# Kernel tuning notes

Hardware: AMD Instinct MI355X
Metric: run time of the kernel (lower is better)

The kernel has to match this reference:

```python
import jax, jax.numpy as jnp
import numpy as np

IMAGE_SIZE = 800
OUT = 50          # feature map size
FEAT = 512
SCALES = (2.0, 4.0, 6.0)
RATIOS = (0.5, 1.0, 1.5)
A = len(SCALES) * len(RATIOS)          # 9 anchors per cell
POS_THR, NEG_THR = 0.7, 0.3
W_CONF, W_REG = 1.0, 5.0
SCALE = IMAGE_SIZE // OUT              # 16, stride of feature map


def _anchor_base():
    # order: ratio outer loop, scale inner loop (matches get_anchor_base)
    ws = jnp.array([s * r for r in RATIOS for s in SCALES], jnp.float32)  # [A]
    hs = jnp.array([s for r in RATIOS for s in SCALES], jnp.float32)      # [A]
    cx = (jnp.arange(OUT, dtype=jnp.float32) + 0.5)[:, None, None]        # grid dim0 -> x
    cy = (jnp.arange(OUT, dtype=jnp.float32) + 0.5)[None, :, None]        # grid dim1 -> y
    xmin = jnp.clip(cx - ws / 2, 0.0, OUT)
    xmax = jnp.clip(cx + ws / 2, 0.0, OUT)
    ymin = jnp.clip(cy - hs / 2, 0.0, OUT)
    ymax = jnp.clip(cy + hs / 2, 0.0, OUT)
    shp = (OUT, OUT, A)
    base = jnp.stack([jnp.broadcast_to(xmin, shp), jnp.broadcast_to(ymin, shp),
                      jnp.broadcast_to(xmax, shp), jnp.broadcast_to(ymax, shp)], axis=-1)
    return base.reshape(-1, 4)         # [N,4], N = OUT*OUT*A = 22500


def _iou(anchors, gt):
    # anchors [N,4], gt [B,M,4] (xyxy) -> iou [B,N,M]
    a = anchors[None, :, None, :]
    g = gt[:, None, :, :]
    ix1 = jnp.maximum(a[..., 0], g[..., 0]); iy1 = jnp.maximum(a[..., 1], g[..., 1])
    ix2 = jnp.minimum(a[..., 2], g[..., 2]); iy2 = jnp.minimum(a[..., 3], g[..., 3])
    inter = jnp.clip(ix2 - ix1, 0.0) * jnp.clip(iy2 - iy1, 0.0)
    area_a = (a[..., 2] - a[..., 0]) * (a[..., 3] - a[..., 1])
    area_g = (g[..., 2] - g[..., 0]) * (g[..., 3] - g[..., 1])
    return inter / (area_a + area_g - inter + 1e-8)


def _smooth_l1(d):
    ad = jnp.abs(d)
    return jnp.where(ad < 1.0, 0.5 * d * d, ad - 0.5)


def setup_inputs() -> dict:
    key = jax.random.key(0)
    ks = jax.random.split(key, 8)
    B, M = 16, 16
    features = jax.random.normal(ks[0], (B, FEAT, OUT, OUT), jnp.float32)
    # valid GT boxes in image coords: centers in [100,700], sizes in [32,200]
    cxy = jax.random.uniform(ks[1], (B, M, 2), jnp.float32, 100.0, 700.0)
    wh = jax.random.uniform(ks[2], (B, M, 2), jnp.float32, 32.0, 200.0)
    x1y1 = jnp.clip(cxy - wh / 2, 0.0, IMAGE_SIZE)
    x2y2 = jnp.clip(cxy + wh / 2, 0.0, IMAGE_SIZE)
    gt_boxes = jnp.concatenate([x1y1, x2y2], axis=-1)
    w1 = jax.random.normal(ks[3], (FEAT, FEAT, 3, 3), jnp.float32) * 0.02
    b1 = jnp.zeros((FEAT,), jnp.float32)
    w_cls = jax.random.normal(ks[4], (A, FEAT), jnp.float32) * 0.02
    b_cls = jnp.zeros((A,), jnp.float32)
    w_box = jax.random.normal(ks[5], (4 * A, FEAT), jnp.float32) * 0.02
    b_box = jnp.zeros((4 * A,), jnp.float32)
    return {"features": features, "gt_boxes": gt_boxes, "w1": w1, "b1": b1,
            "w_cls": w_cls, "b_cls": b_cls, "w_box": w_box, "b_box": b_box}


def reference(features, gt_boxes, w1, b1, w_cls, b_cls, w_box, b_box):
    B = features.shape[0]
    anchors = _anchor_base()                                   # [N,4]
    N = anchors.shape[0]

    # --- conv tower ---
    x = jax.lax.conv_general_dilated(features, w1, (1, 1), 'SAME') + b1[None, :, None, None]
    cls_map = jnp.einsum('bchw,ac->bahw', x, w_cls) + b_cls[None, :, None, None]   # [B,A,H,W]
    box_map = jnp.einsum('bchw,dc->bdhw', x, w_box) + b_box[None, :, None, None]   # [B,4A,H,W]
    logits = jnp.transpose(cls_map, (0, 2, 3, 1)).reshape(B, N)                    # [B,N]
    pred_off = jnp.transpose(box_map.reshape(B, A, 4, OUT, OUT), (0, 3, 4, 1, 2)).reshape(B, N, 4)

    # --- project gt to feature-map (anchor) coords, 'p2a' ---
    gt = gt_boxes / SCALE                                       # [B,M,4]

    # --- anchor/GT assignment ---
    iou = _iou(anchors, gt)                                     # [B,N,M]
    max_per_gt = jnp.max(iou, axis=1, keepdims=True)            # best anchor per gt
    pos_mask = ((iou == max_per_gt) & (max_per_gt > 0)) | (iou > POS_THR)  # [B,N,M]
    pos_mask = pos_mask.astype(jnp.float32)
    n_pos = jnp.maximum(pos_mask.sum(), 1.0)

    # --- gt offsets (standard tx,ty,tw,th) for every (anchor,gt) pair ---
    acx = (anchors[:, 0] + anchors[:, 2]) / 2
    acy = (anchors[:, 1] + anchors[:, 3]) / 2
    aw = jnp.maximum(anchors[:, 2] - anchors[:, 0], 1e-6)
    ah = jnp.maximum(anchors[:, 3] - anchors[:, 1], 1e-6)
    gcx = (gt[..., 0] + gt[..., 2]) / 2                         # [B,M]
    gcy = (gt[..., 1] + gt[..., 3]) / 2
    gw = jnp.maximum(gt[..., 2] - gt[..., 0], 1e-6)
    gh = jnp.maximum(gt[..., 3] - gt[..., 1], 1e-6)
    tx = (gcx[:, None, :] - acx[None, :, None]) / aw[None, :, None]   # [B,N,M]
    ty = (gcy[:, None, :] - acy[None, :, None]) / ah[None, :, None]
    tw = jnp.log(gw[:, None, :] / aw[None, :, None])
    th = jnp.log(gh[:, None, :] / ah[None, :, None])
    gt_off = jnp.stack([tx, ty, tw, th], axis=-1)               # [B,N,M,4]

    diff = gt_off - pred_off[:, :, None, :]
    reg_loss = (pos_mask[..., None] * _smooth_l1(diff)).sum() / (4.0 * n_pos)

    # --- classification loss: BCE-with-logits; positives=1, negatives=0 ---
    pos_loss = (pos_mask * jax.nn.softplus(-logits)[:, :, None]).sum() / n_pos
    neg_anchor = jnp.all(iou < NEG_THR, axis=2).astype(jnp.float32)   # [B,N]
    n_neg = jnp.maximum(neg_anchor.sum(), 1.0)
    neg_loss = (neg_anchor * jax.nn.softplus(logits)).sum() / n_neg
    cls_loss = 0.5 * (pos_loss + neg_loss)

    total_rpn_loss = W_CONF * cls_loss + W_REG * reg_loss

    # --- proposals from predicted offsets for all anchors ---
    pcx = acx[None, :] + pred_off[..., 0] * aw[None, :]
    pcy = acy[None, :] + pred_off[..., 1] * ah[None, :]
    pw = aw[None, :] * jnp.exp(pred_off[..., 2])
    ph = ah[None, :] * jnp.exp(pred_off[..., 3])
    proposals = jnp.stack([pcx - pw / 2, pcy - ph / 2, pcx + pw / 2, pcy + ph / 2], axis=-1)  # [B,N,4]

    return total_rpn_loss, proposals
```

## Files before the change

kernel.cpp:

```cpp
#include <hip/hip_runtime.h>
#include <hip/hip_bf16.h>
#include <stdint.h>


using bf16x8 = __attribute__((ext_vector_type(8))) __bf16;
using f32x4  = __attribute__((ext_vector_type(4))) float;

#define FT_CHUNK_STRIDE 2768896
#define W2_CHUNK_B 27648

__device__ __forceinline__ unsigned short f2bf(float f) {
  union { float f; unsigned u; } x; x.f = f;
  unsigned r = x.u + 0x7fffu + ((x.u >> 16) & 1u);
  return (unsigned short)(r >> 16);
}

__device__ __forceinline__ void gl_lds16(const void* g, void* l) {
  __builtin_amdgcn_global_load_lds(
      (const __attribute__((address_space(1))) void*)g,
      (__attribute__((address_space(3))) void*)l, 16, 0, 0);
}

__device__ __forceinline__ float sl1(float d) {
  float ad = fabsf(d);
  return ad < 1.f ? 0.5f * d * d : ad - 0.5f;
}
__device__ __forceinline__ float softplus_f(float x) {
  return fmaxf(x, 0.f) + log1pf(expf(-fabsf(x)));
}

__device__ __forceinline__ void anchor_strict(int n, float& ax1, float& ay1,
                                              float& ax2, float& ay2) {
  int ii = n / 450;
  int rem = n - ii * 450;
  int jj = rem / 9;
  int a  = rem - jj * 9;
  const float SC[3] = {2.f, 4.f, 6.f};
  const float RA[3] = {0.5f, 1.f, 1.5f};
  float w = __fmul_rn(SC[a % 3], RA[a / 3]);
  float h = SC[a % 3];
  float cx = __fadd_rn((float)ii, 0.5f);
  float cy = __fadd_rn((float)jj, 0.5f);
  float wh = __fmul_rn(w, 0.5f), hh = __fmul_rn(h, 0.5f);
  ax1 = fminf(fmaxf(__fsub_rn(cx, wh), 0.f), 50.f);
  ax2 = fminf(fmaxf(__fadd_rn(cx, wh), 0.f), 50.f);
  ay1 = fminf(fmaxf(__fsub_rn(cy, hh), 0.f), 50.f);
  ay2 = fminf(fmaxf(__fadd_rn(cy, hh), 0.f), 50.f);
}
__device__ __forceinline__ float iou_pre(float ax1, float ay1, float ax2, float ay2,
                                         float aarea, const float* __restrict__ s) {
  float ix1 = fmaxf(ax1, s[0]), iy1 = fmaxf(ay1, s[1]);
  float ix2 = fminf(ax2, s[2]), iy2 = fminf(ay2, s[3]);
  float inter = __fmul_rn(fmaxf(__fsub_rn(ix2, ix1), 0.f),
                          fmaxf(__fsub_rn(iy2, iy1), 0.f));
  float denom = __fadd_rn(__fsub_rn(__fadd_rn(aarea, s[4]), inter), 1e-8f);
  return __fdiv_rn(inter, denom);
}
__device__ __forceinline__ float iou_strict(float ax1, float ay1, float ax2, float ay2,
                                            float aarea, const float* __restrict__ g) {
  float s[5];
  s[0] = __fmul_rn(g[0], 0.0625f); s[1] = __fmul_rn(g[1], 0.0625f);
  s[2] = __fmul_rn(g[2], 0.0625f); s[3] = __fmul_rn(g[3], 0.0625f);
  s[4] = __fmul_rn(__fsub_rn(s[2], s[0]), __fsub_rn(s[3], s[1]));
  return iou_pre(ax1, ay1, ax2, ay2, aarea, s);
}

__global__ __launch_bounds__(256, 4) void k1(const float* __restrict__ feat,
                                             char* __restrict__ featT2,
                                             const float* __restrict__ w1,
                                             const float* __restrict__ wc,
                                             const float* __restrict__ wb,
                                             const float* __restrict__ b1,
                                             const float* __restrict__ bc,
                                             const float* __restrict__ bbx,
                                             float* __restrict__ part,
                                             float* __restrict__ bias_eff,
                                             const float* __restrict__ gt_boxes,
                                             unsigned* __restrict__ mx,
                                             unsigned* __restrict__ accz) {
  __shared__ __align__(16) char smem[64 * 132 * 2];
  const int bxr = blockIdx.x;
  const int tid = threadIdx.x;

  if (bxr < 576) {
    if (bxr == 0 && tid < 8) accz[tid] = 0u;
    int cz = bxr / 72, kx = bxr - cz * 72;
    float* sW = (float*)smem;
#pragma unroll
    for (int q = 0; q < 12; ++q) {
      int idx = tid + q * 256;
      int co = idx >> 6, cl = idx & 63;
      int c = cz * 64 + cl;
      float v = 0.f;
      if (co < 9) v = wc[co * 512 + c];
      else if (co < 45) v = wb[(co - 9) * 512 + c];
      sW[co * 64 + cl] = v;
    }
    __syncthreads();
    const int kmem = kx * 64 + (tid & 63);
    const int coq  = tid >> 6;
    float acc[12];
#pragma unroll
    for (int j = 0; j < 12; ++j) acc[j] = 0.f;
    const float* w1p = w1 + (size_t)(cz * 64) * 4608 + kmem;
    for (int c4 = 0; c4 < 64; c4 += 4) {
      float f0 = w1p[(size_t)(c4 + 0) * 4608];
      float f1 = w1p[(size_t)(c4 + 1) * 4608];
      float f2 = w1p[(size_t)(c4 + 2) * 4608];
      float f3 = w1p[(size_t)(c4 + 3) * 4608];
#pragma unroll
      for (int j = 0; j < 12; ++j) {
        float4 wv = *(const float4*)&sW[(coq * 12 + j) * 64 + c4];
        acc[j] += wv.x * f0 + wv.y * f1 + wv.z * f2 + wv.w * f3;
      }
    }
    float* dst = part + (size_t)cz * 221184 + kmem;
#pragma unroll
    for (int j = 0; j < 12; ++j) dst[(size_t)(coq * 12 + j) * 4608] = acc[j];
    return;
  }

  if (bxr < 624) {
    int co = bxr - 576;
    int l = tid;
    if (l >= 64) return;
    float s = 0.f;
#pragma unroll
    for (int q = 0; q < 8; ++q) {
      int c = q * 64 + l;
      float wv = co < 9 ? wc[co * 512 + c] : (co < 45 ? wb[(co - 9) * 512 + c] : 0.f);
      s += wv * b1[c];
    }
    for (int o = 32; o; o >>= 1) s += __shfl_down(s, o, 64);
    if (l == 0)
      bias_eff[co] = s + (co < 9 ? bc[co] : (co < 45 ? bbx[co - 9] : 0.f));
    return;
  }

  if (bxr < 880) {
    int q = bxr - 624;
    int b = q >> 4, m = q & 15;
    const float* g = gt_boxes + (b * 16 + m) * 4;
    float s[5];
    s[0] = __fmul_rn(g[0], 0.0625f); s[1] = __fmul_rn(g[1], 0.0625f);
    s[2] = __fmul_rn(g[2], 0.0625f); s[3] = __fmul_rn(g[3], 0.0625f);
    s[4] = __fmul_rn(__fsub_rn(s[2], s[0]), __fsub_rn(s[3], s[1]));
    float best = 0.f;
    for (int n = tid; n < 22500; n += 256) {
      float ax1, ay1, ax2, ay2;
      anchor_strict(n, ax1, ay1, ax2, ay2);
      float aarea = __fmul_rn(__fsub_rn(ax2, ax1), __fsub_rn(ay2, ay1));
      best = fmaxf(best, iou_pre(ax1, ay1, ax2, ay2, aarea, s));
    }
    for (int o = 32; o; o >>= 1) best = fmaxf(best, __shfl_down(best, o, 64));
    float* red = (float*)smem;
    if ((tid & 63) == 0) red[tid >> 6] = best;
    __syncthreads();
    if (tid == 0) {
      float v = fmaxf(fmaxf(red[0], red[1]), fmaxf(red[2], red[3]));
      mx[b * 16 + m] = __float_as_uint(v);
    }
    return;
  }

  const int bxr2 = bxr - 880;
  const int tile = bxr2 % 41;
  const int rest = bxr2 / 41;
  const int g    = rest & 3;
  const int b    = rest >> 2;
  if (tile == 40) {
    uint4 z = {0, 0, 0, 0};
    for (int u = tid; u < 204 * 4; u += 256) {
      int p = u & 255; if (p >= 204) p -= 204;
      int c4 = u / 204;
      int ip, jp;
      if (p < 52)       { ip = 0;       jp = p; }
      else if (p < 104) { ip = 51;      jp = p - 52; }
      else if (p < 154) { ip = p - 103; jp = 0; }
      else              { ip = p - 153; jp = 51; }
      char* dst = featT2 + (size_t)(g * 4 + c4) * FT_CHUNK_STRIDE
                + (size_t)(b * 2704 + ip * 52 + jp) * 64;
      *(uint4*)(dst)      = z;
      *(uint4*)(dst + 16) = z;
      *(uint4*)(dst + 32) = z;
      *(uint4*)(dst + 48) = z;
    }
    return;
  }
  unsigned short* sT = (unsigned short*)smem;
  const int pos0 = tile * 64;
  const float* fb = feat + (size_t)b * 1280000 + (size_t)(g * 128) * 2500;
  const int pq = tid & 15;
  const int cq = tid >> 4;
  const int p  = pos0 + pq * 4;
  float vv[2][4][4];
  if (p + 3 < 2500) {
#pragma unroll
    for (int it = 0; it < 2; ++it)
#pragma unroll
      for (int q = 0; q < 4; ++q) {
        float4 v = *(const float4*)(fb + (size_t)(it * 64 + cq * 4 + q) * 2500 + p);
        vv[it][q][0] = v.x; vv[it][q][1] = v.y;
        vv[it][q][2] = v.z; vv[it][q][3] = v.w;
      }
  } else {
#pragma unroll
    for (int it = 0; it < 2; ++it)
#pragma unroll
      for (int q = 0; q < 4; ++q)
#pragma unroll
        for (int e = 0; e < 4; ++e)
          vv[it][q][e] = fb[(size_t)(it * 64 + cq * 4 + q) * 2500 + min(p + e, 2499)];
  }
#pragma unroll
  for (int it = 0; it < 2; ++it) {
#pragma unroll
    for (int pp = 0; pp < 4; ++pp) {
      ushort4 pk;
      pk.x = f2bf(vv[it][0][pp]); pk.y = f2bf(vv[it][1][pp]);
      pk.z = f2bf(vv[it][2][pp]); pk.w = f2bf(vv[it][3][pp]);
      *(ushort4*)&sT[(pq * 4 + pp) * 132 + it * 64 + cq * 4] = pk;
    }
  }
  __syncthreads();
  {
    int ch = tid >> 6, pr = tid & 63;
    int gp = pos0 + pr;
    if (gp < 2500) {
      int i = gp / 50, j = gp - i * 50;
      char* dst = featT2 + (size_t)(g * 4 + ch) * FT_CHUNK_STRIDE
                + (size_t)(b * 2704 + (i + 1) * 52 + (j + 1)) * 64;
      const uint4* src = (const uint4*)&sT[pr * 132 + ch * 32];
      uint4 a0 = src[0], a1 = src[1], a2 = src[2], a3 = src[3];
      *(uint4*)(dst)      = a0;
      *(uint4*)(dst + 16) = a1;
      *(uint4*)(dst + 32) = a2;
      *(uint4*)(dst + 48) = a3;
    }
  }
}

__global__ __launch_bounds__(256) void k2(const float* __restrict__ part,
                                          unsigned short* __restrict__ w2) {
  int co = blockIdx.x / 18, kx = blockIdx.x - co * 18;
  int kmem = kx * 256 + threadIdx.x;
  const float* p = part + (size_t)co * 4608 + kmem;
  float s = 0.f;
#pragma unroll
  for (int cz = 0; cz < 8; ++cz) s += p[(size_t)cz * 221184];
  int ci = kmem / 9, tap = kmem - ci * 9;
  int c = ci >> 5, e = ci & 31;
  int boff = c * W2_CHUNK_B + tap * 3072 + (co >> 4) * 1024 + (co & 15) * 64
           + ((((e >> 3) ^ co) & 3) << 4) + ((e & 7) << 1);
  w2[boff >> 1] = f2bf(s);
}

__global__ __launch_bounds__(256, 2) void k3(const char* __restrict__ featT2,
                                             const char* __restrict__ w2g,
                                             const float* __restrict__ beff,
                                             float* __restrict__ oh) {
  __shared__ __align__(16) char sF[2][11264];
  __shared__ __align__(16) char sA[2][27648];
  const int tid = threadIdx.x, lane = tid & 63, w = tid >> 6;
  const int bx0 = blockIdx.x;
  const int bx = ((bx0 & 7) << 6) | (bx0 >> 3);
  const int b = bx >> 5, tl = bx & 31, tr = tl >> 3, tc = tl & 7;
  const int i0 = tr * 13 - (tr == 3 ? 1 : 0);
  const int TI = (tr >= 2) ? 12 : 13;
  const int TJ = (tc < 2) ? 7 : 6;
  const int j0 = (tc < 2) ? tc * 7 : 14 + (tc - 2) * 6;
  const int TJ2 = TJ + 2;
  const int mcount = TI * TJ;
  const int pieces = (TI + 2) * TJ2 * 5;

  const char* srcF[3];
#pragma unroll
  for (int k = 0; k < 3; ++k) {
    int s = w * 3 + k;
    int pi = s * 64 + lane;
    if (pi >= pieces) pi = pieces - 1;
    int pos = pi / 5, pc = pi - pos * 5;
    if (pc > 3) pc = 3;
    int hi = pos / TJ2, hj = pos - hi * TJ2;
    srcF[k] = featT2 + (size_t)(b * 2704 + (i0 + hi) * 52 + (j0 + hj)) * 64 + pc * 16;
  }
  int idxB[2];
#pragma unroll
  for (int bf = 0; bf < 2; ++bf) {
    int p = (w * 2 + bf) * 16 + (lane & 15);
    if (p >= mcount) p = mcount - 1;
    int di = p / TJ, dj = p - di * TJ;
    idxB[bf] = (di * TJ2 + dj) * 80 + (lane >> 4) * 16;
  }
  const int aoff = (lane & 15) * 64 + ((((lane >> 4) ^ lane) & 3) << 4);
  int toff[9];
#pragma unroll
  for (int tp = 0; tp < 9; ++tp) toff[tp] = ((tp / 3) * TJ2 + (tp % 3)) * 80;

  f32x4 acc[3][2] = {};

  auto stage = [&](int c, int pb) {
    size_t coff = (size_t)c * FT_CHUNK_STRIDE;
#pragma unroll
    for (int k = 0; k < 3; ++k) {
      int s = w * 3 + k;
      if (s < 11) gl_lds16(srcF[k] + coff, sF[pb] + s * 1024);
    }
#pragma unroll
    for (int k = 0; k < 7; ++k) {
      int s = w + 4 * k;
      if (s < 27)
        gl_lds16(w2g + (size_t)c * W2_CHUNK_B + s * 1024 + lane * 16, sA[pb] + s * 1024);
    }
  };

  stage(0, 0);
  __builtin_amdgcn_s_waitcnt(0);
  __syncthreads();

  for (int c = 0; c < 16; ++c) {
    int pb = c & 1;
    if (c < 15) stage(c + 1, pb ^ 1);
    const char* fA = sA[pb];
    const char* fB = sF[pb];
#pragma unroll
    for (int tp = 0; tp < 9; ++tp) {
      bf16x8 av[3], bv[2];
#pragma unroll
      for (int cf = 0; cf < 3; ++cf)
        av[cf] = *(const bf16x8*)(fA + tp * 3072 + cf * 1024 + aoff);
#pragma unroll
      for (int bf = 0; bf < 2; ++bf)
        bv[bf] = *(const bf16x8*)(fB + idxB[bf] + toff[tp]);
#pragma unroll
      for (int cf = 0; cf < 3; ++cf)
#pragma unroll
        for (int bf = 0; bf < 2; ++bf)
          acc[cf][bf] = __builtin_amdgcn_mfma_f32_16x16x32_bf16(av[cf], bv[bf], acc[cf][bf], 0, 0, 0);
    }
    __builtin_amdgcn_s_waitcnt(0);
    __syncthreads();
  }

  f32x4 bias[3];
#pragma unroll
  for (int cf = 0; cf < 3; ++cf)
    bias[cf] = *(const f32x4*)(beff + cf * 16 + (lane >> 4) * 4);
#pragma unroll
  for (int bf = 0; bf < 2; ++bf) {
    int p = (w * 2 + bf) * 16 + (lane & 15);
    if (p >= mcount) continue;
    int di = p / TJ, dj = p - di * TJ;
    int gm = (b * 50 + i0 + di) * 50 + (j0 + dj);
#pragma unroll
    for (int cf = 0; cf < 3; ++cf) {
      f32x4 v = acc[cf][bf];
#pragma unroll
      for (int r = 0; r < 4; ++r) v[r] += bias[cf][r];
      *(f32x4*)(oh + (size_t)gm * 48 + cf * 16 + (lane >> 4) * 4) = v;
    }
  }
}

__global__ __launch_bounds__(256) void k4(const float* __restrict__ gt_boxes,
                                          const unsigned* __restrict__ mxbuf,
                                          const float* __restrict__ oh,
                                          float* __restrict__ accum,
                                          float* __restrict__ dout) {
  const int tid = threadIdx.x;
  const int b = blockIdx.y;
  __shared__ float sg[16][10];
  if (tid < 16) {
    const float* g = gt_boxes + (b * 16 + tid) * 4;
    float gx1 = __fmul_rn(g[0], 0.0625f), gy1 = __fmul_rn(g[1], 0.0625f);
    float gx2 = __fmul_rn(g[2], 0.0625f), gy2 = __fmul_rn(g[3], 0.0625f);
    sg[tid][0] = gx1; sg[tid][1] = gy1; sg[tid][2] = gx2; sg[tid][3] = gy2;
    sg[tid][4] = __fmul_rn(__fsub_rn(gx2, gx1), __fsub_rn(gy2, gy1));
    sg[tid][5] = (gx1 + gx2) * 0.5f;
    sg[tid][6] = (gy1 + gy2) * 0.5f;
    sg[tid][7] = fmaxf(gx2 - gx1, 1e-6f);
    sg[tid][8] = fmaxf(gy2 - gy1, 1e-6f);
  }
  __syncthreads();

  const int n0 = blockIdx.x * 512 + tid;
  const int n1 = n0 + 256;
  const bool vA = n0 < 22500, vB = n1 < 22500;
  float s_np = 0.f, s_reg = 0.f, s_pos = 0.f, s_nc = 0.f, s_nl = 0.f;

  float Aax1 = 0, Aay1 = 0, Aax2 = 0, Aay2 = 0, Aarea = 0, Aacx = 0, Aacy = 0,
        Aaw = 1, Aah = 1, Alog = 0, Ap0 = 0, Ap1 = 0, Ap2 = 0, Ap3 = 0;
  float Bax1 = 0, Bay1 = 0, Bax2 = 0, Bay2 = 0, Barea = 0, Bacx = 0, Bacy = 0,
        Baw = 1, Bah = 1, Blog = 0, Bp0 = 0, Bp1 = 0, Bp2 = 0, Bp3 = 0;
  int npA = 0, npB = 0;
  bool anA = true, anB = true;

  if (vA) {
    anchor_strict(n0, Aax1, Aay1, Aax2, Aay2);
    Aarea = __fmul_rn(__fsub_rn(Aax2, Aax1), __fsub_rn(Aay2, Aay1));
    Aacx = (Aax1 + Aax2) * 0.5f; Aacy = (Aay1 + Aay2) * 0.5f;
    Aaw = fmaxf(Aax2 - Aax1, 1e-6f); Aah = fmaxf(Aay2 - Aay1, 1e-6f);
    int ii = n0 / 450, rem = n0 - ii * 450, jj = rem / 9, a = rem - jj * 9;
    const float* row = oh + ((size_t)(b * 2500 + ii * 50 + jj)) * 48;
    Alog = row[a];
    Ap0 = row[9 + a * 4]; Ap1 = row[10 + a * 4];
    Ap2 = row[11 + a * 4]; Ap3 = row[12 + a * 4];
  }
  if (vB) {
    anchor_strict(n1, Bax1, Bay1, Bax2, Bay2);
    Barea = __fmul_rn(__fsub_rn(Bax2, Bax1), __fsub_rn(Bay2, Bay1));
    Bacx = (Bax1 + Bax2) * 0.5f; Bacy = (Bay1 + Bay2) * 0.5f;
    Baw = fmaxf(Bax2 - Bax1, 1e-6f); Bah = fmaxf(Bay2 - Bay1, 1e-6f);
    int ii = n1 / 450, rem = n1 - ii * 450, jj = rem / 9, a = rem - jj * 9;
    const float* row = oh + ((size_t)(b * 2500 + ii * 50 + jj)) * 48;
    Blog = row[a];
    Bp0 = row[9 + a * 4]; Bp1 = row[10 + a * 4];
    Bp2 = row[11 + a * 4]; Bp3 = row[12 + a * 4];
  }

#pragma unroll
  for (int m = 0; m < 16; ++m) {
    const float* s = sg[m];
    float mxv = __uint_as_float(mxbuf[b * 16 + m]);
    float iouA = vA ? iou_pre(Aax1, Aay1, Aax2, Aay2, Aarea, s) : 0.f;
    float iouB = vB ? iou_pre(Bax1, Bay1, Bax2, Bay2, Barea, s) : 0.f;
    if (vA) {
      bool pos = ((iouA == mxv) && (mxv > 0.f)) || (iouA > 0.7f);
      if (iouA >= 0.3f) anA = false;
      if (pos) {
        ++npA;
        float tx = (s[5] - Aacx) / Aaw, ty = (s[6] - Aacy) / Aah;
        float twv = logf(s[7] / Aaw), thv = logf(s[8] / Aah);
        s_reg += sl1(tx - Ap0) + sl1(ty - Ap1) + sl1(twv - Ap2) + sl1(thv - Ap3);
      }
    }
    if (vB) {
      bool pos = ((iouB == mxv) && (mxv > 0.f)) || (iouB > 0.7f);
      if (iouB >= 0.3f) anB = false;
      if (pos) {
        ++npB;
        float tx = (s[5] - Bacx) / Baw, ty = (s[6] - Bacy) / Bah;
        float twv = logf(s[7] / Baw), thv = logf(s[8] / Bah);
        s_reg += sl1(tx - Bp0) + sl1(ty - Bp1) + sl1(twv - Bp2) + sl1(thv - Bp3);
      }
    }
  }
  if (vA) {
    s_np += (float)npA;
    s_pos += (float)npA * softplus_f(-Alog);
    if (anA) { s_nc += 1.f; s_nl += softplus_f(Alog); }
    float pcx = Aacx + Ap0 * Aaw, pcy = Aacy + Ap1 * Aah;
    float pw = Aaw * expf(Ap2), ph = Aah * expf(Ap3);
    float* o = dout + 1 + ((size_t)b * 22500 + n0) * 4;
    o[0] = pcx - pw * 0.5f; o[1] = pcy - ph * 0.5f;
    o[2] = pcx + pw * 0.5f; o[3] = pcy + ph * 0.5f;
  }
  if (vB) {
    s_np += (float)npB;
    s_pos += (float)npB * softplus_f(-Blog);
    if (anB) { s_nc += 1.f; s_nl += softplus_f(Blog); }
    float pcx = Bacx + Bp0 * Baw, pcy = Bacy + Bp1 * Bah;
    float pw = Baw * expf(Bp2), ph = Bah * expf(Bp3);
    float* o = dout + 1 + ((size_t)b * 22500 + n1) * 4;
    o[0] = pcx - pw * 0.5f; o[1] = pcy - ph * 0.5f;
    o[2] = pcx + pw * 0.5f; o[3] = pcy + ph * 0.5f;
  }

  float vals[5] = {s_np, s_reg, s_pos, s_nc, s_nl};
  __shared__ float red[4][5];
#pragma unroll
  for (int q = 0; q < 5; ++q) {
    float v = vals[q];
    for (int o = 32; o; o >>= 1) v += __shfl_down(v, o, 64);
    if ((tid & 63) == 0) red[tid >> 6][q] = v;
  }
  __syncthreads();
  if (tid < 5) {
    float v = red[0][tid] + red[1][tid] + red[2][tid] + red[3][tid];
    atomicAdd(accum + tid, v);
  }
  __syncthreads();
  if (tid == 0) {
    __threadfence();
    unsigned old = atomicAdd((unsigned*)(accum + 5), 1u);
    if (old == 703u) {
      float np = fmaxf(atomicAdd(accum + 0, 0.f), 1.f);
      float rg = atomicAdd(accum + 1, 0.f);
      float pp = atomicAdd(accum + 2, 0.f);
      float nn = fmaxf(atomicAdd(accum + 3, 0.f), 1.f);
      float nl = atomicAdd(accum + 4, 0.f);
      dout[0] = 0.5f * (pp / np + nl / nn) + 5.f * (rg / (4.f * np));
    }
  }
}

extern "C" void kernel_launch(void* const* d_in, const int* in_sizes, int n_in,
                              void* d_out, int out_size, void* d_ws, size_t ws_size,
                              hipStream_t stream) {
  const float* features = (const float*)d_in[0];
  const float* gt_boxes = (const float*)d_in[1];
  const float* w1    = (const float*)d_in[2];
  const float* b1    = (const float*)d_in[3];
  const float* w_cls = (const float*)d_in[4];
  const float* b_cls = (const float*)d_in[5];
  const float* w_box = (const float*)d_in[6];
  const float* b_box = (const float*)d_in[7];
  float* out = (float*)d_out;
  char* ws = (char*)d_ws;

  char*           featT2 = ws;
  unsigned short* w2     = (unsigned short*)(ws + 44302336);
  float*          wpart  = (float*)(ws + 44855296);
  float*          oh     = (float*)(ws + 51933184);
  float*          beff   = (float*)(ws + 59613184);
  unsigned*       mx     = (unsigned*)(ws + 59613376);
  float*          accum  = (float*)(ws + 59614400);

  k1<<<3504, 256, 0, stream>>>(features, featT2, w1, w_cls, w_box, b1, b_cls,
                               b_box, wpart, beff, gt_boxes, mx,
                               (unsigned*)accum);
  k2<<<864, 256, 0, stream>>>(wpart, w2);
  k3<<<512, 256, 0, stream>>>(featT2, (const char*)w2, beff, oh);
  k4<<<dim3(44, 16), 256, 0, stream>>>(gt_boxes, mx, oh, accum, out);
}
```

Baseline: 238.1 us.

## Split feature transpose into separate kernel with direct register-to-global bf16 writes

```diff
diff --git a/kernel.cpp b/kernel.cpp
--- a/kernel.cpp
+++ b/kernel.cpp
@@ -56,36 +56,81 @@
   float denom = __fadd_rn(__fsub_rn(__fadd_rn(aarea, s[4]), inter), 1e-8f);
   return __fdiv_rn(inter, denom);
 }
-__device__ __forceinline__ float iou_strict(float ax1, float ay1, float ax2, float ay2,
-                                            float aarea, const float* __restrict__ g) {
-  float s[5];
-  s[0] = __fmul_rn(g[0], 0.0625f); s[1] = __fmul_rn(g[1], 0.0625f);
-  s[2] = __fmul_rn(g[2], 0.0625f); s[3] = __fmul_rn(g[3], 0.0625f);
-  s[4] = __fmul_rn(__fsub_rn(s[2], s[0]), __fsub_rn(s[3], s[1]));
-  return iou_pre(ax1, ay1, ax2, ay2, aarea, s);
-}
-
-__global__ __launch_bounds__(256, 4) void k1(const float* __restrict__ feat,
-                                             char* __restrict__ featT2,
-                                             const float* __restrict__ w1,
-                                             const float* __restrict__ wc,
-                                             const float* __restrict__ wb,
-                                             const float* __restrict__ b1,
-                                             const float* __restrict__ bc,
-                                             const float* __restrict__ bbx,
-                                             float* __restrict__ part,
-                                             float* __restrict__ bias_eff,
-                                             const float* __restrict__ gt_boxes,
-                                             unsigned* __restrict__ mx,
-                                             unsigned* __restrict__ accz) {
-  __shared__ __align__(16) char smem[64 * 132 * 2];
+
+__global__ __launch_bounds__(256, 4) void k1a(const float* __restrict__ feat,
+                                              char* __restrict__ featT2) {
+  const int bx = blockIdx.x;
+  const int tid = threadIdx.x;
+  if (bx >= 768) {
+    int q = bx - 768;
+    int c = q & 15, b = q >> 4;
+    uint4 z = {0, 0, 0, 0};
+    for (int p = tid; p < 204; p += 256) {
+      int ip, jp;
+      if (p < 52)       { ip = 0;       jp = p; }
+      else if (p < 104) { ip = 51;      jp = p - 52; }
+      else if (p < 154) { ip = p - 103; jp = 0; }
+      else              { ip = p - 153; jp = 51; }
+      char* dst = featT2 + (size_t)c * FT_CHUNK_STRIDE
+                + (size_t)(b * 2704 + ip * 52 + jp) * 64;
+      *(uint4*)(dst)      = z;
+      *(uint4*)(dst + 16) = z;
+      *(uint4*)(dst + 32) = z;
+      *(uint4*)(dst + 48) = z;
+    }
+    return;
+  }
+  const int t = bx % 3, rest = bx / 3;
+  const int c = rest & 15, b = rest >> 4;
+  const int p0 = t * 1024 + tid * 4;
+  if (p0 >= 2500) return;
+  const float* fb = feat + (size_t)b * 1280000 + (size_t)(c * 32) * 2500 + p0;
+  char* d[4];
+#pragma unroll
+  for (int pp = 0; pp < 4; ++pp) {
+    int gp = p0 + pp;
+    int i = gp / 50, j = gp - i * 50;
+    d[pp] = featT2 + (size_t)c * FT_CHUNK_STRIDE
+          + (size_t)(b * 2704 + (i + 1) * 52 + (j + 1)) * 64;
+  }
+#pragma unroll
+  for (int h = 0; h < 2; ++h) {
+    float4 v[16];
+#pragma unroll
+    for (int q = 0; q < 16; ++q)
+      v[q] = *(const float4*)(fb + (size_t)(h * 16 + q) * 2500);
+#pragma unroll
+    for (int pp = 0; pp < 4; ++pp) {
+      unsigned short u[16];
+#pragma unroll
+      for (int q = 0; q < 16; ++q) {
+        float fv = pp == 0 ? v[q].x : pp == 1 ? v[q].y : pp == 2 ? v[q].z : v[q].w;
+        u[q] = f2bf(fv);
+      }
+      *(uint4*)(d[pp] + h * 32)      = *(uint4*)&u[0];
+      *(uint4*)(d[pp] + h * 32 + 16) = *(uint4*)&u[8];
+    }
+  }
+}
+
+__global__ __launch_bounds__(256, 4) void k1b(const float* __restrict__ w1,
+                                              const float* __restrict__ wc,
+                                              const float* __restrict__ wb,
+                                              const float* __restrict__ b1,
+                                              const float* __restrict__ bc,
+                                              const float* __restrict__ bbx,
+                                              float* __restrict__ part,
+                                              float* __restrict__ bias_eff,
+                                              const float* __restrict__ gt_boxes,
+                                              unsigned* __restrict__ mx,
+                                              unsigned* __restrict__ accz) {
+  __shared__ __align__(16) float sW[48 * 64];
   const int bxr = blockIdx.x;
   const int tid = threadIdx.x;
 
   if (bxr < 576) {
     if (bxr == 0 && tid < 8) accz[tid] = 0u;
     int cz = bxr / 72, kx = bxr - cz * 72;
-    float* sW = (float*)smem;
 #pragma unroll
     for (int q = 0; q < 12; ++q) {
       int idx = tid + q * 256;
@@ -137,7 +182,7 @@
     return;
   }
 
-  if (bxr < 880) {
+  {
     int q = bxr - 624;
     int b = q >> 4, m = q & 15;
     const float* g = gt_boxes + (b * 16 + m) * 4;
@@ -153,89 +198,11 @@
       best = fmaxf(best, iou_pre(ax1, ay1, ax2, ay2, aarea, s));
     }
     for (int o = 32; o; o >>= 1) best = fmaxf(best, __shfl_down(best, o, 64));
-    float* red = (float*)smem;
-    if ((tid & 63) == 0) red[tid >> 6] = best;
+    if ((tid & 63) == 0) sW[tid >> 6] = best;
     __syncthreads();
     if (tid == 0) {
-      float v = fmaxf(fmaxf(red[0], red[1]), fmaxf(red[2], red[3]));
+      float v = fmaxf(fmaxf(sW[0], sW[1]), fmaxf(sW[2], sW[3]));
       mx[b * 16 + m] = __float_as_uint(v);
-    }
-    return;
-  }
-
-  const int bxr2 = bxr - 880;
-  const int tile = bxr2 % 41;
-  const int rest = bxr2 / 41;
-  const int g    = rest & 3;
-  const int b    = rest >> 2;
-  if (tile == 40) {
-    uint4 z = {0, 0, 0, 0};
-    for (int u = tid; u < 204 * 4; u += 256) {
-      int p = u & 255; if (p >= 204) p -= 204;
-      int c4 = u / 204;
-      int ip, jp;
-      if (p < 52)       { ip = 0;       jp = p; }
-      else if (p < 104) { ip = 51;      jp = p - 52; }
-      else if (p < 154) { ip = p - 103; jp = 0; }
-      else              { ip = p - 153; jp = 51; }
-      char* dst = featT2 + (size_t)(g * 4 + c4) * FT_CHUNK_STRIDE
-                + (size_t)(b * 2704 + ip * 52 + jp) * 64;
-      *(uint4*)(dst)      = z;
-      *(uint4*)(dst + 16) = z;
-      *(uint4*)(dst + 32) = z;
-      *(uint4*)(dst + 48) = z;
-    }
-    return;
-  }
-  unsigned short* sT = (unsigned short*)smem;
-  const int pos0 = tile * 64;
-  const float* fb = feat + (size_t)b * 1280000 + (size_t)(g * 128) * 2500;
-  const int pq = tid & 15;
-  const int cq = tid >> 4;
-  const int p  = pos0 + pq * 4;
-  float vv[2][4][4];
-  if (p + 3 < 2500) {
-#pragma unroll
-    for (int it = 0; it < 2; ++it)
-#pragma unroll
-      for (int q = 0; q < 4; ++q) {
-        float4 v = *(const float4*)(fb + (size_t)(it * 64 + cq * 4 + q) * 2500 + p);
-        vv[it][q][0] = v.x; vv[it][q][1] = v.y;
-        vv[it][q][2] = v.z; vv[it][q][3] = v.w;
-      }
-  } else {
-#pragma unroll
-    for (int it = 0; it < 2; ++it)
-#pragma unroll
-      for (int q = 0; q < 4; ++q)
-#pragma unroll
-        for (int e = 0; e < 4; ++e)
-          vv[it][q][e] = fb[(size_t)(it * 64 + cq * 4 + q) * 2500 + min(p + e, 2499)];
-  }
-#pragma unroll
-  for (int it = 0; it < 2; ++it) {
-#pragma unroll
-    for (int pp = 0; pp < 4; ++pp) {
-      ushort4 pk;
-      pk.x = f2bf(vv[it][0][pp]); pk.y = f2bf(vv[it][1][pp]);
-      pk.z = f2bf(vv[it][2][pp]); pk.w = f2bf(vv[it][3][pp]);
-      *(ushort4*)&sT[(pq * 4 + pp) * 132 + it * 64 + cq * 4] = pk;
-    }
-  }
-  __syncthreads();
-  {
-    int ch = tid >> 6, pr = tid & 63;
-    int gp = pos0 + pr;
-    if (gp < 2500) {
-      int i = gp / 50, j = gp - i * 50;
-      char* dst = featT2 + (size_t)(g * 4 + ch) * FT_CHUNK_STRIDE
-                + (size_t)(b * 2704 + (i + 1) * 52 + (j + 1)) * 64;
-      const uint4* src = (const uint4*)&sT[pr * 132 + ch * 32];
-      uint4 a0 = src[0], a1 = src[1], a2 = src[2], a3 = src[3];
-      *(uint4*)(dst)      = a0;
-      *(uint4*)(dst + 16) = a1;
-      *(uint4*)(dst + 32) = a2;
-      *(uint4*)(dst + 48) = a3;
     }
   }
 }
@@ -516,10 +483,10 @@
   unsigned*       mx     = (unsigned*)(ws + 59613376);
   float*          accum  = (float*)(ws + 59614400);
 
-  k1<<<3504, 256, 0, stream>>>(features, featT2, w1, w_cls, w_box, b1, b_cls,
-                               b_box, wpart, beff, gt_boxes, mx,
-                               (unsigned*)accum);
+  k1b<<<880, 256, 0, stream>>>(w1, w_cls, w_box, b1, b_cls, b_box, wpart, beff,
+                               gt_boxes, mx, (unsigned*)accum);
   k2<<<864, 256, 0, stream>>>(wpart, w2);
+  k1a<<<1024, 256, 0, stream>>>(features, featT2);
   k3<<<512, 256, 0, stream>>>(featT2, (const char*)w2, beff, oh);
   k4<<<dim3(44, 16), 256, 0, stream>>>(gt_boxes, mx, oh, accum, out);
 }
```

New measurement: 270.4 us. +13.6%, slower.

## Split per-GT max-IoU search across anchor chunks with two-stage reduction

Applied to the files above, without the earlier changes.

```diff
diff --git a/kernel.cpp b/kernel.cpp
--- a/kernel.cpp
+++ b/kernel.cpp
@@ -56,14 +56,6 @@
   float denom = __fadd_rn(__fsub_rn(__fadd_rn(aarea, s[4]), inter), 1e-8f);
   return __fdiv_rn(inter, denom);
 }
-__device__ __forceinline__ float iou_strict(float ax1, float ay1, float ax2, float ay2,
-                                            float aarea, const float* __restrict__ g) {
-  float s[5];
-  s[0] = __fmul_rn(g[0], 0.0625f); s[1] = __fmul_rn(g[1], 0.0625f);
-  s[2] = __fmul_rn(g[2], 0.0625f); s[3] = __fmul_rn(g[3], 0.0625f);
-  s[4] = __fmul_rn(__fsub_rn(s[2], s[0]), __fsub_rn(s[3], s[1]));
-  return iou_pre(ax1, ay1, ax2, ay2, aarea, s);
-}
 
 __global__ __launch_bounds__(256, 4) void k1(const float* __restrict__ feat,
                                              char* __restrict__ featT2,
@@ -76,9 +68,9 @@
                                              float* __restrict__ part,
                                              float* __restrict__ bias_eff,
                                              const float* __restrict__ gt_boxes,
-                                             unsigned* __restrict__ mx,
+                                             float* __restrict__ mxPart,
                                              unsigned* __restrict__ accz) {
-  __shared__ __align__(16) char smem[64 * 132 * 2];
+  __shared__ __align__(16) char smem[16896];
   const int bxr = blockIdx.x;
   const int tid = threadIdx.x;
 
@@ -137,33 +129,47 @@
     return;
   }
 
-  if (bxr < 880) {
+  if (bxr < 2032) {
     int q = bxr - 624;
-    int b = q >> 4, m = q & 15;
-    const float* g = gt_boxes + (b * 16 + m) * 4;
-    float s[5];
-    s[0] = __fmul_rn(g[0], 0.0625f); s[1] = __fmul_rn(g[1], 0.0625f);
-    s[2] = __fmul_rn(g[2], 0.0625f); s[3] = __fmul_rn(g[3], 0.0625f);
-    s[4] = __fmul_rn(__fsub_rn(s[2], s[0]), __fsub_rn(s[3], s[1]));
-    float best = 0.f;
-    for (int n = tid; n < 22500; n += 256) {
+    int b = q / 88, nb = q - b * 88;
+    int n = nb * 256 + tid;
+    float (*sgg)[5] = (float(*)[5])smem;
+    float (*red)[16] = (float(*)[16])((float*)smem + 128);
+    if (tid < 16) {
+      const float* g = gt_boxes + (b * 16 + tid) * 4;
+      float gx1 = __fmul_rn(g[0], 0.0625f), gy1 = __fmul_rn(g[1], 0.0625f);
+      float gx2 = __fmul_rn(g[2], 0.0625f), gy2 = __fmul_rn(g[3], 0.0625f);
+      sgg[tid][0] = gx1; sgg[tid][1] = gy1; sgg[tid][2] = gx2; sgg[tid][3] = gy2;
+      sgg[tid][4] = __fmul_rn(__fsub_rn(gx2, gx1), __fsub_rn(gy2, gy1));
+    }
+    __syncthreads();
+    float lm[16];
+#pragma unroll
+    for (int m = 0; m < 16; ++m) lm[m] = 0.f;
+    if (n < 22500) {
       float ax1, ay1, ax2, ay2;
       anchor_strict(n, ax1, ay1, ax2, ay2);
       float aarea = __fmul_rn(__fsub_rn(ax2, ax1), __fsub_rn(ay2, ay1));
-      best = fmaxf(best, iou_pre(ax1, ay1, ax2, ay2, aarea, s));
-    }
-    for (int o = 32; o; o >>= 1) best = fmaxf(best, __shfl_down(best, o, 64));
-    float* red = (float*)smem;
-    if ((tid & 63) == 0) red[tid >> 6] = best;
+#pragma unroll
+      for (int m = 0; m < 16; ++m)
+        lm[m] = iou_pre(ax1, ay1, ax2, ay2, aarea, sgg[m]);
+    }
+#pragma unroll
+    for (int m = 0; m < 16; ++m) {
+      float v = lm[m];
+      for (int o = 32; o; o >>= 1) v = fmaxf(v, __shfl_down(v, o, 64));
+      if ((tid & 63) == 0) red[tid >> 6][m] = v;
+    }
     __syncthreads();
-    if (tid == 0) {
-      float v = fmaxf(fmaxf(red[0], red[1]), fmaxf(red[2], red[3]));
-      mx[b * 16 + m] = __float_as_uint(v);
+    if (tid < 16) {
+      float v = fmaxf(fmaxf(red[0][tid], red[1][tid]),
+                      fmaxf(red[2][tid], red[3][tid]));
+      mxPart[(b * 16 + tid) * 88 + nb] = v;
     }
     return;
   }
 
-  const int bxr2 = bxr - 880;
+  const int bxr2 = bxr - 2032;
   const int tile = bxr2 % 41;
   const int rest = bxr2 / 41;
   const int g    = rest & 3;
@@ -241,7 +247,17 @@
 }
 
 __global__ __launch_bounds__(256) void k2(const float* __restrict__ part,
-                                          unsigned short* __restrict__ w2) {
+                                          unsigned short* __restrict__ w2,
+                                          const float* __restrict__ mxPart,
+                                          unsigned* __restrict__ mx) {
+  if (blockIdx.x == 864) {
+    int t = threadIdx.x;
+    const float* mp = mxPart + t * 88;
+    float v = 0.f;
+    for (int k = 0; k < 88; ++k) v = fmaxf(v, mp[k]);
+    mx[t] = __float_as_uint(v);
+    return;
+  }
   int co = blockIdx.x / 18, kx = blockIdx.x - co * 18;
   int kmem = kx * 256 + threadIdx.x;
   const float* p = part + (size_t)co * 4608 + kmem;
@@ -380,6 +396,7 @@
     sg[tid][6] = (gy1 + gy2) * 0.5f;
     sg[tid][7] = fmaxf(gx2 - gx1, 1e-6f);
     sg[tid][8] = fmaxf(gy2 - gy1, 1e-6f);
+    sg[tid][9] = __uint_as_float(mxbuf[b * 16 + tid]);
   }
   __syncthreads();
 
@@ -421,7 +438,7 @@
 #pragma unroll
   for (int m = 0; m < 16; ++m) {
     const float* s = sg[m];
-    float mxv = __uint_as_float(mxbuf[b * 16 + m]);
+    float mxv = s[9];
     float iouA = vA ? iou_pre(Aax1, Aay1, Aax2, Aay2, Aarea, s) : 0.f;
     float iouB = vB ? iou_pre(Bax1, Bay1, Bax2, Bay2, Barea, s) : 0.f;
     if (vA) {
@@ -513,13 +530,14 @@
   float*          wpart  = (float*)(ws + 44855296);
   float*          oh     = (float*)(ws + 51933184);
   float*          beff   = (float*)(ws + 59613184);
-  unsigned*       mx     = (unsigned*)(ws + 59613376);
-  float*          accum  = (float*)(ws + 59614400);
-
-  k1<<<3504, 256, 0, stream>>>(features, featT2, w1, w_cls, w_box, b1, b_cls,
-                               b_box, wpart, beff, gt_boxes, mx,
+  float*          mxPart = (float*)(ws + 59613376);
+  unsigned*       mx     = (unsigned*)(ws + 59703488);
+  float*          accum  = (float*)(ws + 59704512);
+
+  k1<<<4656, 256, 0, stream>>>(features, featT2, w1, w_cls, w_box, b1, b_cls,
+                               b_box, wpart, beff, gt_boxes, mxPart,
                                (unsigned*)accum);
-  k2<<<864, 256, 0, stream>>>(wpart, w2);
+  k2<<<865, 256, 0, stream>>>(wpart, w2, mxPart, mx);
   k3<<<512, 256, 0, stream>>>(featT2, (const char*)w2, beff, oh);
   k4<<<dim3(44, 16), 256, 0, stream>>>(gt_boxes, mx, oh, accum, out);
 }
```

Result: slower. 247.8 us (+4.1%).
